# Kernel optimization log

Measured on AMD Instinct MI355X. Metric: run time of the kernel, lower is better.

## Reference

```python
import jax, jax.numpy as jnp
import numpy as np

N = 100000      # nodes
E = 1600000     # edges (avg degree 16)
DIN, DH, DOUT = 128, 128, 64


def setup_inputs() -> dict:
    key = jax.random.key(0)
    k0, k1, k2, k3 = jax.random.split(key, 4)
    x = jax.random.normal(k0, (N, DIN), jnp.float32)
    edge_index = jax.random.randint(k1, (2, E), 0, N, dtype=jnp.int64)
    W1 = jax.random.normal(k2, (DIN, DH), jnp.float32) / np.sqrt(DIN).astype(np.float32)
    b1 = jnp.zeros((DH,), jnp.float32)
    W2 = jax.random.normal(k3, (DH, DOUT), jnp.float32) / np.sqrt(DH).astype(np.float32)
    b2 = jnp.zeros((DOUT,), jnp.float32)
    return {"x": x, "edge_index": edge_index, "W1": W1, "b1": b1, "W2": W2, "b2": b2}


def reference(x, edge_index, W1, b1, W2, b2):
    n = x.shape[0]
    # PyG GCNConv: add self-loops, symmetric normalization deg^-1/2 A_hat deg^-1/2
    loops = jnp.arange(n, dtype=edge_index.dtype)
    src = jnp.concatenate([edge_index[0], loops])  # message sources
    dst = jnp.concatenate([edge_index[1], loops])  # aggregation targets
    deg = jax.ops.segment_sum(jnp.ones(src.shape, x.dtype), dst, num_segments=n)
    dinv = jnp.where(deg > 0, jax.lax.rsqrt(deg), 0.0)
    norm = dinv[src] * dinv[dst]                    # [E+N]

    def gcn_conv(h, W, b):
        h = h @ W                                   # dense transform first (PyG order)
        msg = h[src] * norm[:, None]                # gather + scale
        return jax.ops.segment_sum(msg, dst, num_segments=n) + b

    h = jax.nn.relu(gcn_conv(x, W1, b1))
    # F.dropout is identity in eval mode (self.training == False)
    return gcn_conv(h, W2, b2)
```

## Files before the change

kernel.cpp:

```cpp
#include <hip/hip_runtime.h>

#define DIN 128
#define DH  128
#define DOUT 64

typedef __attribute__((ext_vector_type(8))) short bf16x8;
typedef __attribute__((ext_vector_type(4))) float f32x4;


__device__ inline unsigned bf16rne(float f) {
    unsigned u = __float_as_uint(f);
    return (u + 0x7fffu + ((u >> 16) & 1u)) >> 16;
}

__device__ inline void acc8(float* a, uint4 v) {
    a[0] += __uint_as_float(v.x << 16); a[1] += __uint_as_float(v.x & 0xffff0000u);
    a[2] += __uint_as_float(v.y << 16); a[3] += __uint_as_float(v.y & 0xffff0000u);
    a[4] += __uint_as_float(v.z << 16); a[5] += __uint_as_float(v.z & 0xffff0000u);
    a[6] += __uint_as_float(v.w << 16); a[7] += __uint_as_float(v.w & 0xffff0000u);
}


__global__ void k_count_rank(const int* __restrict__ dst, int* __restrict__ cnt,
                             int* __restrict__ rank, int E, int pad) {
    int e = blockIdx.x * 256 + threadIdx.x;
    if (e < E) rank[e] = atomicAdd(&cnt[dst[e] * pad], 1);
}

__global__ void k_dinv(const int* __restrict__ cnt, float* __restrict__ dinv, int n, int pad) {
    int i = blockIdx.x * 256 + threadIdx.x;
    if (i < n) dinv[i] = rsqrtf((float)(cnt[i * pad] + 1));
}

__global__ void k_scan_partial(const int* __restrict__ cnt, int* __restrict__ excl,
                               int* __restrict__ bsum, int n, int pad) {
    __shared__ int sd[256];
    int t = threadIdx.x;
    int base = blockIdx.x * 1024 + t * 4;
    int v0 = (base + 0 < n) ? cnt[(base + 0) * pad] : 0;
    int v1 = (base + 1 < n) ? cnt[(base + 1) * pad] : 0;
    int v2 = (base + 2 < n) ? cnt[(base + 2) * pad] : 0;
    int v3 = (base + 3 < n) ? cnt[(base + 3) * pad] : 0;
    int s = v0 + v1 + v2 + v3;
    sd[t] = s;
    __syncthreads();
    for (int off = 1; off < 256; off <<= 1) {
        int x = (t >= off) ? sd[t - off] : 0;
        __syncthreads();
        sd[t] += x;
        __syncthreads();
    }
    int incl = sd[t];
    if (t == 255) bsum[blockIdx.x] = incl;
    int run = incl - s;
    if (base + 0 < n) excl[base + 0] = run;  run += v0;
    if (base + 1 < n) excl[base + 1] = run;  run += v1;
    if (base + 2 < n) excl[base + 2] = run;  run += v2;
    if (base + 3 < n) excl[base + 3] = run;
}

__global__ void k_scan_bsum(int* __restrict__ bsum, int nb) {
    __shared__ int sd[256];
    int t = threadIdx.x;
    int v = (t < nb) ? bsum[t] : 0;
    sd[t] = v;
    __syncthreads();
    for (int off = 1; off < 256; off <<= 1) {
        int x = (t >= off) ? sd[t - off] : 0;
        __syncthreads();
        sd[t] += x;
        __syncthreads();
    }
    if (t < nb) bsum[t] = sd[t] - v;
}

__global__ void k_finalize(int* __restrict__ rowstart, const int* __restrict__ bsum,
                           int n, int E) {
    int i = blockIdx.x * 256 + threadIdx.x;
    if (i < n) rowstart[i] += bsum[i >> 10];
    if (i == 0) rowstart[n] = E;
}

__global__ void k_fill2(const int* __restrict__ src, const int* __restrict__ dst,
                        const int* __restrict__ rank, const int* __restrict__ rowstart,
                        int* __restrict__ adj, int E) {
    int e = blockIdx.x * 256 + threadIdx.x;
    if (e < E) adj[rowstart[dst[e]] + rank[e]] = src[e];
}


__global__ void k_wsplit(const float* __restrict__ W, unsigned short* __restrict__ Wt_hi,
                         unsigned short* __restrict__ Wt_lo, int N) {
    int idx = blockIdx.x * 256 + threadIdx.x;
    if (idx >= N * 128) return;
    int n = idx >> 7;
    int k = idx & 127;
    float v = W[(size_t)k * N + n];
    unsigned h = bf16rne(v);
    float hf = __uint_as_float(h << 16);
    unsigned l = bf16rne(v - hf);
    Wt_hi[idx] = (unsigned short)h;
    Wt_lo[idx] = (unsigned short)l;
}


template <int NCOLS>
__global__ void k_gemm_mfma(const float* __restrict__ A,
                            const unsigned short* __restrict__ Wt_hi,
                            const unsigned short* __restrict__ Wt_lo,
                            const float* __restrict__ dinv,
                            unsigned short* __restrict__ S, int M) {
    constexpr int NT = NCOLS / 16;
    int wave = threadIdx.x >> 6;
    int lane = threadIdx.x & 63;
    int row0 = blockIdx.x * 64 + wave * 16;
    int arow = row0 + (lane & 15);
    if (arow >= M) arow = M - 1;
    int kfrag = (lane >> 4) * 8;
    int bcol = lane & 15;

    f32x4 acc[NT];
    #pragma unroll
    for (int t = 0; t < NT; t++) acc[t] = (f32x4){0.f, 0.f, 0.f, 0.f};

    #pragma unroll
    for (int ks = 0; ks < 4; ks++) {
        const float* ap = A + (size_t)arow * 128 + ks * 32 + kfrag;
        float4 av0 = *(const float4*)ap;
        float4 av1 = *(const float4*)(ap + 4);
        float av[8] = {av0.x, av0.y, av0.z, av0.w, av1.x, av1.y, av1.z, av1.w};
        bf16x8 ahi, alo;
        #pragma unroll
        for (int j = 0; j < 8; j++) {
            unsigned h = bf16rne(av[j]);
            float hf = __uint_as_float(h << 16);
            ahi[j] = (short)h;
            alo[j] = (short)bf16rne(av[j] - hf);
        }
        #pragma unroll
        for (int t = 0; t < NT; t++) {
            size_t boff = (size_t)(t * 16 + bcol) * 128 + ks * 32 + kfrag;
            bf16x8 bhi = *(const bf16x8*)(Wt_hi + boff);
            bf16x8 blo = *(const bf16x8*)(Wt_lo + boff);
            acc[t] = __builtin_amdgcn_mfma_f32_16x16x32_bf16(ahi, bhi, acc[t], 0, 0, 0);
            acc[t] = __builtin_amdgcn_mfma_f32_16x16x32_bf16(ahi, blo, acc[t], 0, 0, 0);
            acc[t] = __builtin_amdgcn_mfma_f32_16x16x32_bf16(alo, bhi, acc[t], 0, 0, 0);
        }
    }

    int srow0 = row0 + (lane >> 4) * 4;
    #pragma unroll
    for (int r = 0; r < 4; r++) {
        int row = srow0 + r;
        if (row < M) {
            float dv = dinv[row];
            #pragma unroll
            for (int t = 0; t < NT; t++)
                S[(size_t)row * NCOLS + t * 16 + bcol] = (unsigned short)bf16rne(dv * acc[t][r]);
        }
    }
}


template <bool RELU>
__global__ void k_agg128(const unsigned short* __restrict__ S, const int* __restrict__ rowstart,
                         const int* __restrict__ adj, const float* __restrict__ dinv,
                         const float* __restrict__ bias, float* __restrict__ out, int n) {
    int wave = threadIdx.x >> 6;
    int lane = threadIdx.x & 63;
    int node = blockIdx.x * 4 + wave;
    if (node >= n) return;
    int start = rowstart[node];
    int end   = rowstart[node + 1];
    int g  = lane >> 4;
    int fo = lane & 15;

    const uint4* S4 = (const uint4*)S;
    float a0[8] = {}, a1[8] = {};

    while (start < end) {
        int cnt = end - start;
        if (cnt > 64) cnt = 64;
        int nb = adj[start + (lane < cnt ? lane : cnt - 1)];
        int t = 0;
        for (; t + 16 <= cnt; t += 16) {
            int jA = __shfl(nb, t + 0  + g);
            int jB = __shfl(nb, t + 4  + g);
            int jC = __shfl(nb, t + 8  + g);
            int jD = __shfl(nb, t + 12 + g);
            uint4 mA = S4[(size_t)jA * 16 + fo];
            uint4 mB = S4[(size_t)jB * 16 + fo];
            uint4 mC = S4[(size_t)jC * 16 + fo];
            uint4 mD = S4[(size_t)jD * 16 + fo];
            acc8(a0, mA); acc8(a1, mB); acc8(a0, mC); acc8(a1, mD);
        }
        for (; t + 4 <= cnt; t += 4) {
            int j = __shfl(nb, t + g);
            uint4 m = S4[(size_t)j * 16 + fo];
            acc8(a0, m);
        }
        if (t < cnt) {
            int i1 = t + g;
            int j = __shfl(nb, i1 < cnt ? i1 : cnt - 1);
            uint4 m = S4[(size_t)j * 16 + fo];
            if (i1 < cnt) acc8(a1, m);
        }
        start += 64;
    }

    float acc[8];
    #pragma unroll
    for (int i = 0; i < 8; i++) {
        float v = a0[i] + a1[i];
        v += __shfl_xor(v, 16);
        v += __shfl_xor(v, 32);
        acc[i] = v;
    }

    uint4 selfu = ((const uint4*)S)[(size_t)node * 16 + fo];
    float self[8] = {};
    acc8(self, selfu);
    float dv = dinv[node];
    float4 bb0 = ((const float4*)bias)[fo * 2 + 0];
    float4 bb1 = ((const float4*)bias)[fo * 2 + 1];
    float o[8];
    o[0] = dv * (acc[0] + self[0]) + bb0.x;
    o[1] = dv * (acc[1] + self[1]) + bb0.y;
    o[2] = dv * (acc[2] + self[2]) + bb0.z;
    o[3] = dv * (acc[3] + self[3]) + bb0.w;
    o[4] = dv * (acc[4] + self[4]) + bb1.x;
    o[5] = dv * (acc[5] + self[5]) + bb1.y;
    o[6] = dv * (acc[6] + self[6]) + bb1.z;
    o[7] = dv * (acc[7] + self[7]) + bb1.w;
    if (RELU) {
        #pragma unroll
        for (int i = 0; i < 8; i++) o[i] = fmaxf(o[i], 0.f);
    }
    if (g == 0) {
        float4* op = (float4*)(out + (size_t)node * 128 + fo * 8);
        op[0] = make_float4(o[0], o[1], o[2], o[3]);
        op[1] = make_float4(o[4], o[5], o[6], o[7]);
    }
}

__global__ void k_agg64(const unsigned short* __restrict__ S, const int* __restrict__ rowstart,
                        const int* __restrict__ adj, const float* __restrict__ dinv,
                        const float* __restrict__ bias, float* __restrict__ out, int n) {
    int wave = threadIdx.x >> 6;
    int lane = threadIdx.x & 63;
    int node = blockIdx.x * 4 + wave;
    if (node >= n) return;
    int start = rowstart[node];
    int end   = rowstart[node + 1];
    int g  = lane >> 3;
    int fo = lane & 7;

    const uint4* S4 = (const uint4*)S;
    float a0[8] = {}, a1[8] = {};

    while (start < end) {
        int cnt = end - start;
        if (cnt > 64) cnt = 64;
        int nb = adj[start + (lane < cnt ? lane : cnt - 1)];
        int t = 0;
        for (; t + 32 <= cnt; t += 32) {
            int jA = __shfl(nb, t + 0  + g);
            int jB = __shfl(nb, t + 8  + g);
            int jC = __shfl(nb, t + 16 + g);
            int jD = __shfl(nb, t + 24 + g);
            uint4 mA = S4[(size_t)jA * 8 + fo];
            uint4 mB = S4[(size_t)jB * 8 + fo];
            uint4 mC = S4[(size_t)jC * 8 + fo];
            uint4 mD = S4[(size_t)jD * 8 + fo];
            acc8(a0, mA); acc8(a1, mB); acc8(a0, mC); acc8(a1, mD);
        }
        for (; t + 8 <= cnt; t += 8) {
            int j = __shfl(nb, t + g);
            uint4 m = S4[(size_t)j * 8 + fo];
            acc8(a0, m);
        }
        if (t < cnt) {
            int i1 = t + g;
            int j = __shfl(nb, i1 < cnt ? i1 : cnt - 1);
            uint4 m = S4[(size_t)j * 8 + fo];
            if (i1 < cnt) acc8(a1, m);
        }
        start += 64;
    }

    float acc[8];
    #pragma unroll
    for (int i = 0; i < 8; i++) {
        float v = a0[i] + a1[i];
        v += __shfl_xor(v, 8);
        v += __shfl_xor(v, 16);
        v += __shfl_xor(v, 32);
        acc[i] = v;
    }

    uint4 selfu = ((const uint4*)S)[(size_t)node * 8 + fo];
    float self[8] = {};
    acc8(self, selfu);
    float dv = dinv[node];
    float4 bb0 = ((const float4*)bias)[fo * 2 + 0];
    float4 bb1 = ((const float4*)bias)[fo * 2 + 1];
    float o[8];
    o[0] = dv * (acc[0] + self[0]) + bb0.x;
    o[1] = dv * (acc[1] + self[1]) + bb0.y;
    o[2] = dv * (acc[2] + self[2]) + bb0.z;
    o[3] = dv * (acc[3] + self[3]) + bb0.w;
    o[4] = dv * (acc[4] + self[4]) + bb1.x;
    o[5] = dv * (acc[5] + self[5]) + bb1.y;
    o[6] = dv * (acc[6] + self[6]) + bb1.z;
    o[7] = dv * (acc[7] + self[7]) + bb1.w;
    if (g == 0) {
        float4* op = (float4*)(out + (size_t)node * 64 + fo * 8);
        op[0] = make_float4(o[0], o[1], o[2], o[3]);
        op[1] = make_float4(o[4], o[5], o[6], o[7]);
    }
}


extern "C" void kernel_launch(void* const* d_in, const int* in_sizes, int n_in,
                              void* d_out, int out_size, void* d_ws, size_t ws_size,
                              hipStream_t stream) {
    const float* x  = (const float*)d_in[0];
    const int*   ei = (const int*)d_in[1];
    const float* W1 = (const float*)d_in[2];
    const float* b1 = (const float*)d_in[3];
    const float* W2 = (const float*)d_in[4];
    const float* b2 = (const float*)d_in[5];
    float* out = (float*)d_out;

    int N = in_sizes[0] / DIN;
    int E = in_sizes[1] / 2;
    const int* esrc = ei;
    const int* edst = ei + E;

    size_t fixed = (size_t)N * 128 * 2
                 + (size_t)N * 128 * 4
                 + (size_t)N * 4
                 + (size_t)(N + 1) * 4
                 + (size_t)E * 4 * 2
                 + (128 + 64) * 128 * 2 * 2
                 + 1024 * 4 + 16 * 256;
    int PAD = (fixed + (size_t)N * 16 * 4 <= ws_size) ? 16 : 1;

    char* wsb = (char*)d_ws;
    size_t off = 0;
    auto alloc = [&](size_t bytes) {
        void* p = wsb + off;
        off = (off + bytes + 255) & ~(size_t)255;
        return p;
    };
    unsigned short* S = (unsigned short*)alloc((size_t)N * 128 * 2);
    float* H1       = (float*)alloc((size_t)N * 128 * 4);
    float* dinv     = (float*)alloc((size_t)N * 4);
    int*   rowstart = (int*)alloc((size_t)(N + 1) * 4);
    int*   adj      = (int*)alloc((size_t)E * 4);
    int*   rank     = (int*)alloc((size_t)E * 4);
    unsigned short* wt1h = (unsigned short*)alloc(128 * 128 * 2);
    unsigned short* wt1l = (unsigned short*)alloc(128 * 128 * 2);
    unsigned short* wt2h = (unsigned short*)alloc(64 * 128 * 2);
    unsigned short* wt2l = (unsigned short*)alloc(64 * 128 * 2);
    int*   cnt      = (int*)alloc((size_t)N * PAD * 4);
    int*   bsum     = (int*)alloc(1024 * 4);

    int eb = (E + 255) / 256;
    int nb = (N + 255) / 256;
    int sb = (N + 1023) / 1024;

    k_wsplit<<<(128 * 128) / 256, 256, 0, stream>>>(W1, wt1h, wt1l, 128);
    k_wsplit<<<(64 * 128) / 256, 256, 0, stream>>>(W2, wt2h, wt2l, 64);

    hipMemsetAsync(cnt, 0, (size_t)N * PAD * 4, stream);
    k_count_rank<<<eb, 256, 0, stream>>>(edst, cnt, rank, E, PAD);
    k_dinv<<<nb, 256, 0, stream>>>(cnt, dinv, N, PAD);
    k_scan_partial<<<sb, 256, 0, stream>>>(cnt, rowstart, bsum, N, PAD);
    k_scan_bsum<<<1, 256, 0, stream>>>(bsum, sb);
    k_finalize<<<nb, 256, 0, stream>>>(rowstart, bsum, N, E);
    k_fill2<<<eb, 256, 0, stream>>>(esrc, edst, rank, rowstart, adj, E);

    int gb = (N + 63) / 64;
    int ab = (N + 3) / 4;

    k_gemm_mfma<128><<<gb, 256, 0, stream>>>(x, wt1h, wt1l, dinv, S, N);
    k_agg128<true><<<ab, 256, 0, stream>>>(S, rowstart, adj, dinv, b1, H1, N);

    k_gemm_mfma<64><<<gb, 256, 0, stream>>>(H1, wt2h, wt2l, dinv, S, N);
    k_agg64<<<ab, 256, 0, stream>>>(S, rowstart, adj, dinv, b2, out, N);
}
```

Before: 312.8 us.

## Stage pre-swizzled weight fragments in LDS with persistent GEMM blocks

Weights are pre-split into hi/lo bf16 parts and stored in MFMA fragment order, so each lane reads a contiguous 16-byte fragment. Each GEMM block copies these fragments once into shared memory and then loops persistently over row chunks, with the grid capped at 512 blocks. The kernel also hoists all A loads ahead of the MFMA loop and packs bf16 output pairs through a lane shuffle into 32-bit stores. This targets repeated global weight fetches and narrow 16-bit stores. In exchange it uses up to 64KB of LDS per block, which limits occupancy.

```diff
diff --git a/kernel.cpp b/kernel.cpp
--- a/kernel.cpp
+++ b/kernel.cpp
@@ -89,74 +89,107 @@
 }
 
 
-__global__ void k_wsplit(const float* __restrict__ W, unsigned short* __restrict__ Wt_hi,
-                         unsigned short* __restrict__ Wt_lo, int N) {
+__global__ void k_wsplit_frag(const float* __restrict__ W, unsigned short* __restrict__ Wf_hi,
+                              unsigned short* __restrict__ Wf_lo, int N) {
     int idx = blockIdx.x * 256 + threadIdx.x;
     if (idx >= N * 128) return;
-    int n = idx >> 7;
-    int k = idx & 127;
+    int f = idx >> 9;
+    int r = idx & 511;
+    int lane = r >> 3;
+    int j = r & 7;
+    int t = f >> 2;
+    int ks = f & 3;
+    int n = t * 16 + (lane & 15);
+    int k = ks * 32 + (lane >> 4) * 8 + j;
     float v = W[(size_t)k * N + n];
     unsigned h = bf16rne(v);
     float hf = __uint_as_float(h << 16);
     unsigned l = bf16rne(v - hf);
-    Wt_hi[idx] = (unsigned short)h;
-    Wt_lo[idx] = (unsigned short)l;
+    Wf_hi[idx] = (unsigned short)h;
+    Wf_lo[idx] = (unsigned short)l;
 }
 
 
 template <int NCOLS>
-__global__ void k_gemm_mfma(const float* __restrict__ A,
-                            const unsigned short* __restrict__ Wt_hi,
-                            const unsigned short* __restrict__ Wt_lo,
-                            const float* __restrict__ dinv,
-                            unsigned short* __restrict__ S, int M) {
+__global__ __launch_bounds__(256, 2) void k_gemm_mfma(
+        const float* __restrict__ A,
+        const unsigned short* __restrict__ Wf_hi,
+        const unsigned short* __restrict__ Wf_lo,
+        const float* __restrict__ dinv,
+        unsigned short* __restrict__ S, int M, int nchunks) {
     constexpr int NT = NCOLS / 16;
-    int wave = threadIdx.x >> 6;
-    int lane = threadIdx.x & 63;
-    int row0 = blockIdx.x * 64 + wave * 16;
-    int arow = row0 + (lane & 15);
-    if (arow >= M) arow = M - 1;
+    constexpr int NFRAG = NT * 4;
+    __shared__ unsigned short lh[NFRAG * 512];
+    __shared__ unsigned short ll[NFRAG * 512];
+    int tid = threadIdx.x;
+    constexpr int NV = NFRAG * 512 * 2 / 16;
+    #pragma unroll
+    for (int i = 0; i < NV / 256; i++) {
+        int s = tid + i * 256;
+        ((uint4*)lh)[s] = ((const uint4*)Wf_hi)[s];
+        ((uint4*)ll)[s] = ((const uint4*)Wf_lo)[s];
+    }
+    __syncthreads();
+
+    int wave = tid >> 6;
+    int lane = tid & 63;
     int kfrag = (lane >> 4) * 8;
     int bcol = lane & 15;
-
-    f32x4 acc[NT];
-    #pragma unroll
-    for (int t = 0; t < NT; t++) acc[t] = (f32x4){0.f, 0.f, 0.f, 0.f};
-
-    #pragma unroll
-    for (int ks = 0; ks < 4; ks++) {
-        const float* ap = A + (size_t)arow * 128 + ks * 32 + kfrag;
-        float4 av0 = *(const float4*)ap;
-        float4 av1 = *(const float4*)(ap + 4);
-        float av[8] = {av0.x, av0.y, av0.z, av0.w, av1.x, av1.y, av1.z, av1.w};
-        bf16x8 ahi, alo;
+    const unsigned short* lhp = lh + lane * 8;
+    const unsigned short* llp = ll + lane * 8;
+
+    for (int chunk = blockIdx.x; chunk < nchunks; chunk += gridDim.x) {
+        int row0 = chunk * 64 + wave * 16;
+        int arow = row0 + (lane & 15);
+        if (arow >= M) arow = M - 1;
+        const float* ap = A + (size_t)arow * 128 + kfrag;
+
+        float4 av[4][2];
         #pragma unroll
-        for (int j = 0; j < 8; j++) {
-            unsigned h = bf16rne(av[j]);
-            float hf = __uint_as_float(h << 16);
-            ahi[j] = (short)h;
-            alo[j] = (short)bf16rne(av[j] - hf);
-        }
+        for (int ks = 0; ks < 4; ks++) {
+            av[ks][0] = *(const float4*)(ap + ks * 32);
+            av[ks][1] = *(const float4*)(ap + ks * 32 + 4);
+        }
+
+        f32x4 acc[NT];
         #pragma unroll
-        for (int t = 0; t < NT; t++) {
-            size_t boff = (size_t)(t * 16 + bcol) * 128 + ks * 32 + kfrag;
-            bf16x8 bhi = *(const bf16x8*)(Wt_hi + boff);
-            bf16x8 blo = *(const bf16x8*)(Wt_lo + boff);
-            acc[t] = __builtin_amdgcn_mfma_f32_16x16x32_bf16(ahi, bhi, acc[t], 0, 0, 0);
-            acc[t] = __builtin_amdgcn_mfma_f32_16x16x32_bf16(ahi, blo, acc[t], 0, 0, 0);
-            acc[t] = __builtin_amdgcn_mfma_f32_16x16x32_bf16(alo, bhi, acc[t], 0, 0, 0);
-        }
-    }
-
-    int srow0 = row0 + (lane >> 4) * 4;
-    #pragma unroll
-    for (int r = 0; r < 4; r++) {
-        int row = srow0 + r;
-        if (row < M) {
-            float dv = dinv[row];
+        for (int t = 0; t < NT; t++) acc[t] = (f32x4){0.f, 0.f, 0.f, 0.f};
+
+        #pragma unroll
+        for (int ks = 0; ks < 4; ks++) {
+            float a8[8] = {av[ks][0].x, av[ks][0].y, av[ks][0].z, av[ks][0].w,
+                           av[ks][1].x, av[ks][1].y, av[ks][1].z, av[ks][1].w};
+            bf16x8 ahi, alo;
             #pragma unroll
-            for (int t = 0; t < NT; t++)
-                S[(size_t)row * NCOLS + t * 16 + bcol] = (unsigned short)bf16rne(dv * acc[t][r]);
+            for (int j = 0; j < 8; j++) {
+                unsigned h = bf16rne(a8[j]);
+                float hf = __uint_as_float(h << 16);
+                ahi[j] = (short)h;
+                alo[j] = (short)bf16rne(a8[j] - hf);
+            }
+            #pragma unroll
+            for (int t = 0; t < NT; t++) {
+                int f = t * 4 + ks;
+                bf16x8 bhi = *(const bf16x8*)(lhp + f * 512);
+                bf16x8 blo = *(const bf16x8*)(llp + f * 512);
+                acc[t] = __builtin_amdgcn_mfma_f32_16x16x32_bf16(ahi, bhi, acc[t], 0, 0, 0);
+                acc[t] = __builtin_amdgcn_mfma_f32_16x16x32_bf16(ahi, blo, acc[t], 0, 0, 0);
+                acc[t] = __builtin_amdgcn_mfma_f32_16x16x32_bf16(alo, bhi, acc[t], 0, 0, 0);
+            }
+        }
+
+        int srow0 = row0 + (lane >> 4) * 4;
+        #pragma unroll
+        for (int r = 0; r < 4; r++) {
+            int row = srow0 + r;
+            float dv = (row < M) ? dinv[row] : 0.f;
+            #pragma unroll
+            for (int t = 0; t < NT; t++) {
+                unsigned o = bf16rne(dv * acc[t][r]);
+                unsigned p = (unsigned)__shfl_xor((int)o, 1);
+                if ((lane & 1) == 0 && row < M)
+                    *(unsigned*)(S + (size_t)row * NCOLS + t * 16 + bcol) = o | (p << 16);
+            }
         }
     }
 }
@@ -359,10 +392,10 @@
     int*   rowstart = (int*)alloc((size_t)(N + 1) * 4);
     int*   adj      = (int*)alloc((size_t)E * 4);
     int*   rank     = (int*)alloc((size_t)E * 4);
-    unsigned short* wt1h = (unsigned short*)alloc(128 * 128 * 2);
-    unsigned short* wt1l = (unsigned short*)alloc(128 * 128 * 2);
-    unsigned short* wt2h = (unsigned short*)alloc(64 * 128 * 2);
-    unsigned short* wt2l = (unsigned short*)alloc(64 * 128 * 2);
+    unsigned short* wf1h = (unsigned short*)alloc(128 * 128 * 2);
+    unsigned short* wf1l = (unsigned short*)alloc(128 * 128 * 2);
+    unsigned short* wf2h = (unsigned short*)alloc(64 * 128 * 2);
+    unsigned short* wf2l = (unsigned short*)alloc(64 * 128 * 2);
     int*   cnt      = (int*)alloc((size_t)N * PAD * 4);
     int*   bsum     = (int*)alloc(1024 * 4);
 
@@ -370,8 +403,8 @@
     int nb = (N + 255) / 256;
     int sb = (N + 1023) / 1024;
 
-    k_wsplit<<<(128 * 128) / 256, 256, 0, stream>>>(W1, wt1h, wt1l, 128);
-    k_wsplit<<<(64 * 128) / 256, 256, 0, stream>>>(W2, wt2h, wt2l, 64);
+    k_wsplit_frag<<<(128 * 128) / 256, 256, 0, stream>>>(W1, wf1h, wf1l, 128);
+    k_wsplit_frag<<<(64 * 128) / 256, 256, 0, stream>>>(W2, wf2h, wf2l, 64);
 
     hipMemsetAsync(cnt, 0, (size_t)N * PAD * 4, stream);
     k_count_rank<<<eb, 256, 0, stream>>>(edst, cnt, rank, E, PAD);
@@ -381,12 +414,13 @@
     k_finalize<<<nb, 256, 0, stream>>>(rowstart, bsum, N, E);
     k_fill2<<<eb, 256, 0, stream>>>(esrc, edst, rank, rowstart, adj, E);
 
-    int gb = (N + 63) / 64;
+    int nchunks = (N + 63) / 64;
+    int gb = nchunks < 512 ? nchunks : 512;
     int ab = (N + 3) / 4;
 
-    k_gemm_mfma<128><<<gb, 256, 0, stream>>>(x, wt1h, wt1l, dinv, S, N);
+    k_gemm_mfma<128><<<gb, 256, 0, stream>>>(x, wf1h, wf1l, dinv, S, N, nchunks);
     k_agg128<true><<<ab, 256, 0, stream>>>(S, rowstart, adj, dinv, b1, H1, N);
 
-    k_gemm_mfma<64><<<gb, 256, 0, stream>>>(H1, wt2h, wt2l, dinv, S, N);
+    k_gemm_mfma<64><<<gb, 256, 0, stream>>>(H1, wf2h, wf2l, dinv, S, N, nchunks);
     k_agg64<<<ab, 256, 0, stream>>>(S, rowstart, adj, dinv, b2, out, N);
 }
```

New measurement: 279.8 us. 1.12x faster.
